# Kernel tuning notes

Measured on AMD Instinct MI355X. Metric: run time of the kernel, lower is better.

Reference implementation:

```python
import jax, jax.numpy as jnp
import numpy as np
import math

EMBED = 512
KDIM = 512
VDIM = 512
H = 8
HD = EMBED // H
N = 2048
L = 2048
B = 4


def setup_inputs() -> dict:
    key = jax.random.key(0)
    ks = jax.random.split(key, 14)
    s = 1.0 / math.sqrt(EMBED)
    return {
        "q": jax.random.normal(ks[0], (N, B, EMBED), jnp.float32),
        "k": jax.random.normal(ks[1], (L, B, KDIM), jnp.float32),
        "v": jax.random.normal(ks[2], (L, B, VDIM), jnp.float32),
        "pe1": jax.random.normal(ks[3], (B, N, 3), jnp.float32),
        "pe2": jax.random.normal(ks[4], (L, 3), jnp.float32),
        "Wq": jax.random.normal(ks[5], (EMBED, EMBED), jnp.float32) * s,
        "bq": jnp.zeros((EMBED,), jnp.float32),
        "Wk": jax.random.normal(ks[6], (EMBED, KDIM), jnp.float32) * s,
        "bk": jnp.zeros((EMBED,), jnp.float32),
        "Wv": jax.random.normal(ks[7], (EMBED, VDIM), jnp.float32) * s,
        "bv": jnp.zeros((EMBED,), jnp.float32),
        "Wo": jax.random.normal(ks[8], (EMBED, EMBED), jnp.float32) * s,
        "bo": jnp.zeros((EMBED,), jnp.float32),
    }


def reference(q, k, v, pe1, pe2, Wq, bq, Wk, bk, Wv, bv, Wo, bo):
    n, b, _ = q.shape
    l = k.shape[0]
    # projections (nn.Linear: x @ W.T + b)
    qp = q @ Wq.T + bq  # (n, b, E)
    kp = k @ Wk.T + bk  # (l, b, E)
    vp = v @ Wv.T + bv  # (l, b, E)
    # split heads -> (b, H, n, hd)
    qh = qp.reshape(n, b, H, HD).transpose(1, 2, 0, 3)
    kh = kp.reshape(l, b, H, HD).transpose(1, 2, 0, 3)
    vh = vp.reshape(l, b, H, HD).transpose(1, 2, 0, 3)
    # relative PE bias: (b, n, l), broadcast over heads
    pe_scores = jnp.einsum('bnc,lc->bnl', pe1, pe2)[:, None, :, :]
    scores = (jnp.einsum('bhnd,bhld->bhnl', qh, kh) + pe_scores) / math.sqrt(HD)
    attn = jax.nn.softmax(scores, axis=-1)
    out = jnp.einsum('bhnl,bhld->bhnd', attn, vh)  # (b, H, n, hd)
    out = out.transpose(2, 0, 1, 3).reshape(n, b, EMBED)
    return out @ Wo.T + bo
```

## Files before the change

kernel.cpp:

```cpp
#include <hip/hip_runtime.h>
#include <math.h>

#define EMBED 512
#define HDIM 64
#define NHEADS 8
#define SEQ_N 2048
#define SEQ_L 2048
#define BATCH 4
#define MROWS (SEQ_N*BATCH)
#define BE (BATCH*EMBED)

#define QSCALE 0.18033688f

typedef _Float16 f16;
typedef _Float16 half8 __attribute__((ext_vector_type(8)));
typedef _Float16 half4 __attribute__((ext_vector_type(4)));
typedef _Float16 half2v __attribute__((ext_vector_type(2)));
typedef float floatx4 __attribute__((ext_vector_type(4)));
typedef float floatx16 __attribute__((ext_vector_type(16)));

static __device__ inline float fast_exp2(float x) {
#if __has_builtin(__builtin_amdgcn_exp2f)
  return __builtin_amdgcn_exp2f(x);
#else
  return __expf(x * 0.69314718056f);
#endif
}

static __device__ inline half2v pk2(float a, float b) {
#if __has_builtin(__builtin_amdgcn_cvt_pkrtz)
  return __builtin_bit_cast(half2v, __builtin_amdgcn_cvt_pkrtz(a, b));
#else
  half2v o; o[0] = (f16)a; o[1] = (f16)b; return o;
#endif
}

static __device__ inline void gload16(const void* g, void* l) {
  __builtin_amdgcn_global_load_lds(
      (__attribute__((address_space(1))) void*)(g),
      (__attribute__((address_space(3))) void*)(l), 16, 0, 0);
}

__global__ __launch_bounds__(256) void cvt_all(const float* __restrict__ q,
                                               const float* __restrict__ k,
                                               const float* __restrict__ v,
                                               const float* __restrict__ Wq,
                                               const float* __restrict__ Wk,
                                               const float* __restrict__ Wv,
                                               const float* __restrict__ Wo,
                                               f16* __restrict__ qb, f16* __restrict__ kb,
                                               f16* __restrict__ vb, f16* __restrict__ Wb) {
  const long TOK = (long)MROWS * EMBED;
  const long WSZ = (long)EMBED * EMBED;
  int y = blockIdx.y;
  long i = ((long)blockIdx.x * 256 + threadIdx.x) * 4;
  if (y < 3) {
    if (i < TOK) {
      const float* s = y == 0 ? q : y == 1 ? k : v;
      f16* d = y == 0 ? qb : y == 1 ? kb : vb;
      float4 f = *reinterpret_cast<const float4*>(s + i);
      half4 o; o[0] = (f16)f.x; o[1] = (f16)f.y; o[2] = (f16)f.z; o[3] = (f16)f.w;
      *reinterpret_cast<half4*>(d + i) = o;
    }
  } else {
    if (i < 4 * WSZ) {
      int sel = (int)(i >> 18);
      long off = i & (WSZ - 1);
      const float* s = sel == 0 ? Wq : sel == 1 ? Wk : sel == 2 ? Wv : Wo;
      float4 f = *reinterpret_cast<const float4*>(s + off);
      half4 o; o[0] = (f16)f.x; o[1] = (f16)f.y; o[2] = (f16)f.z; o[3] = (f16)f.w;
      *reinterpret_cast<half4*>(Wb + i) = o;
    }
  }
}

__global__ __launch_bounds__(256) void gemm_qkv(const f16* __restrict__ A0,
                                                const f16* __restrict__ A1,
                                                const f16* __restrict__ A2,
                                                const f16* __restrict__ W0,
                                                const f16* __restrict__ W1,
                                                const f16* __restrict__ W2,
                                                const float* __restrict__ b0,
                                                const float* __restrict__ b1,
                                                const float* __restrict__ b2,
                                                f16* __restrict__ C0, f16* __restrict__ C1,
                                                f16* __restrict__ C2t) {
  __shared__ alignas(16) f16 As[128 * 32];
  __shared__ alignas(16) f16 Bs[128 * 32];
  const int sel = blockIdx.y >> 2;
  const f16* A = sel == 0 ? A0 : sel == 1 ? A1 : A2;
  const f16* Bt = sel == 0 ? W0 : sel == 1 ? W1 : W2;
  const float* bias = sel == 0 ? b0 : sel == 1 ? b1 : b2;
  const float scl = sel == 0 ? QSCALE : 1.0f;
  const int tid = threadIdx.x;
  const int wave = tid >> 6, lane = tid & 63, quad = lane >> 4, l16 = lane & 15;
  const int wm = wave & 1, wn = wave >> 1;
  const long m0 = (long)blockIdx.x * 128;
  const long n0 = (long)(blockIdx.y & 3) * 128;
  floatx4 acc[4][4] = {};
  const int srow = lane >> 2;
  const int scol = (lane & 3) * 8;

  for (int k0 = 0; k0 < EMBED; k0 += 32) {
    __syncthreads();
    gload16(A + (m0 + wave * 32 + srow) * EMBED + k0 + scol, &As[(wave * 32) * 32]);
    gload16(A + (m0 + wave * 32 + 16 + srow) * EMBED + k0 + scol, &As[(wave * 32 + 16) * 32]);
    gload16(Bt + (n0 + wave * 32 + srow) * EMBED + k0 + scol, &Bs[(wave * 32) * 32]);
    gload16(Bt + (n0 + wave * 32 + 16 + srow) * EMBED + k0 + scol, &Bs[(wave * 32 + 16) * 32]);
    __syncthreads();
    half8 af[4], bf[4];
#pragma unroll
    for (int i = 0; i < 4; ++i)
      af[i] = *reinterpret_cast<const half8*>(&As[(wm * 64 + i * 16 + l16) * 32 + quad * 8]);
#pragma unroll
    for (int j = 0; j < 4; ++j)
      bf[j] = *reinterpret_cast<const half8*>(&Bs[(wn * 64 + j * 16 + l16) * 32 + quad * 8]);
#pragma unroll
    for (int i = 0; i < 4; ++i)
#pragma unroll
      for (int j = 0; j < 4; ++j)
        acc[i][j] = __builtin_amdgcn_mfma_f32_16x16x32_f16(af[i], bf[j], acc[i][j], 0, 0, 0);
  }
#pragma unroll
  for (int i = 0; i < 4; ++i)
#pragma unroll
    for (int r = 0; r < 4; ++r) {
      long row = m0 + wm * 64 + i * 16 + quad * 4 + r;
#pragma unroll
      for (int j = 0; j < 4; ++j) {
        long col = n0 + wn * 64 + j * 16 + l16;
        float val = (acc[i][j][r] + bias[col]) * scl;
        if (sel == 2) {
          long bq = row & 3, ltok = row >> 2;
          long hh = col >> 6, dd = col & 63;
          C2t[(((bq << 3) + hh) * 64 + dd) * 2048 + ltok] = (f16)val;
        } else {
          f16* C = sel == 0 ? C0 : C1;
          C[row * EMBED + col] = (f16)val;
        }
      }
    }
}

__global__ __launch_bounds__(256) void gemm_out(const f16* __restrict__ A,
                                                const f16* __restrict__ Bt,
                                                const float* __restrict__ bias,
                                                float* __restrict__ C) {
  __shared__ alignas(16) f16 As[128 * 32];
  __shared__ alignas(16) f16 Bs[64 * 32];
  const int tid = threadIdx.x;
  const int wave = tid >> 6, lane = tid & 63, quad = lane >> 4, l16 = lane & 15;
  const long m0 = (long)blockIdx.x * 128;
  const long n0 = (long)blockIdx.y * 64;
  floatx4 acc[2][4] = {};
  const int srow = lane >> 2;
  const int scol = (lane & 3) * 8;

  for (int k0 = 0; k0 < EMBED; k0 += 32) {
    __syncthreads();
    gload16(A + (m0 + wave * 32 + srow) * EMBED + k0 + scol, &As[(wave * 32) * 32]);
    gload16(A + (m0 + wave * 32 + 16 + srow) * EMBED + k0 + scol, &As[(wave * 32 + 16) * 32]);
    gload16(Bt + (n0 + wave * 16 + srow) * EMBED + k0 + scol, &Bs[(wave * 16) * 32]);
    __syncthreads();
    half8 af[2], bf[4];
#pragma unroll
    for (int i = 0; i < 2; ++i)
      af[i] = *reinterpret_cast<const half8*>(&As[(wave * 32 + i * 16 + l16) * 32 + quad * 8]);
#pragma unroll
    for (int j = 0; j < 4; ++j)
      bf[j] = *reinterpret_cast<const half8*>(&Bs[(j * 16 + l16) * 32 + quad * 8]);
#pragma unroll
    for (int i = 0; i < 2; ++i)
#pragma unroll
      for (int j = 0; j < 4; ++j)
        acc[i][j] = __builtin_amdgcn_mfma_f32_16x16x32_f16(af[i], bf[j], acc[i][j], 0, 0, 0);
  }
#pragma unroll
  for (int i = 0; i < 2; ++i)
#pragma unroll
    for (int r = 0; r < 4; ++r) {
      long row = m0 + wave * 32 + i * 16 + quad * 4 + r;
#pragma unroll
      for (int j = 0; j < 4; ++j) {
        long col = n0 + j * 16 + l16;
        C[row * EMBED + col] = acc[i][j][r] + bias[col];
      }
    }
}

#define KST 88
#define VST 136
#define NCHUNK (SEQ_L / 128)
#define LDSB (128 * KST * 2 + 64 * VST * 2)
__global__ __launch_bounds__(512, 4) void attn_flash(const f16* __restrict__ qp,
                                                     const f16* __restrict__ kp,
                                                     const f16* __restrict__ vt,
                                                     const float* __restrict__ pe1,
                                                     const float* __restrict__ pe2,
                                                     f16* __restrict__ ao) {
  __shared__ alignas(16) unsigned char smem[LDSB];
  f16* Ks = reinterpret_cast<f16*>(smem);
  f16* Vt = reinterpret_cast<f16*>(smem + 128 * KST * 2);
  float* comb = reinterpret_cast<float*>(smem);
  const int tid = threadIdx.x, wave = tid >> 6, lane = tid & 63;
  const int m = lane & 31, h = lane >> 5;
  const int strip = wave & 3, half = wave >> 2;
  const int n0 = blockIdx.x * 128;
  const int b = blockIdx.y >> 3, hd = blockIdx.y & 7;
  const long headoff = (long)b * EMBED + hd * HDIM;
  const long vhead = (long)blockIdx.y * 64 * 2048;

  for (int c = tid; c < 1024; c += 512) {
    int r = c >> 3, col = (c & 7) * 8;
    *reinterpret_cast<uint4*>(&Ks[r * KST + col]) =
        *reinterpret_cast<const uint4*>(qp + (long)(n0 + r) * BE + headoff + col);
    int rv = c >> 4, cv = (c & 15) * 8;
    *reinterpret_cast<uint4*>(&Vt[rv * VST + cv]) =
        *reinterpret_cast<const uint4*>(vt + vhead + (long)rv * 2048 + 0 + cv);
  }
  {
    const uint4 z4 = {0, 0, 0, 0};
    const uint2 z2 = {0, 0};
    int r = tid >> 2, s = tid & 3;
    if (s == 0) *reinterpret_cast<uint2*>(&Ks[r * KST + 68]) = z2;
    else if (s == 1) *reinterpret_cast<uint4*>(&Ks[r * KST + 72]) = z4;
    else if (s == 2) *reinterpret_cast<uint4*>(&Ks[r * KST + 80]) = z4;
  }
  if (tid < 128) {
    long base = ((long)b * SEQ_N + n0 + tid) * 3;
    half4 v8;
    v8[0] = (f16)(pe1[base + 0] * QSCALE);
    v8[1] = (f16)(pe1[base + 1] * QSCALE);
    v8[2] = (f16)(pe1[base + 2] * QSCALE);
    v8[3] = (f16)0.f;
    *reinterpret_cast<half4*>(&Ks[tid * KST + 64]) = v8;
  }
  __syncthreads();

  half8 qf[5];
#pragma unroll
  for (int e = 0; e < 5; ++e)
    qf[e] = *reinterpret_cast<const half8*>(&Ks[(strip * 32 + m) * KST + e * 16 + h * 8]);
  __syncthreads();

  for (int c = tid; c < 1024; c += 512) {
    int r = c >> 3, col = (c & 7) * 8;
    *reinterpret_cast<uint4*>(&Ks[r * KST + col]) =
        *reinterpret_cast<const uint4*>(kp + (long)(0 + r) * BE + headoff + col);
  }
  if (tid < 128) {
    long bb = (long)(0 + tid) * 3;
    half4 p2;
    p2[0] = (f16)pe2[bb + 0]; p2[1] = (f16)pe2[bb + 1];
    p2[2] = (f16)pe2[bb + 2]; p2[3] = (f16)0.f;
    *reinterpret_cast<half4*>(&Ks[tid * KST + 64]) = p2;
  }

  floatx16 oacc[2] = {};
  float lpart = 0.f;

#pragma unroll 1
  for (int c = 0; c < NCHUNK; ++c) {
    __syncthreads();
#pragma unroll
    for (int tt = 0; tt < 2; ++tt) {
      const int t = half * 2 + tt;
      floatx16 st = {};
#pragma unroll
      for (int e = 0; e < 5; ++e) {
        half8 kf = *reinterpret_cast<const half8*>(&Ks[(t * 32 + m) * KST + e * 16 + h * 8]);
        st = __builtin_amdgcn_mfma_f32_32x32x16_f16(kf, qf[e], st, 0, 0, 0);
      }
      float p[16];
#pragma unroll
      for (int r = 0; r < 16; ++r) {
        p[r] = fast_exp2(st[r]);
        lpart += p[r];
      }
#pragma unroll
      for (int s = 0; s < 4; ++s) {
        half2v u0 = pk2(p[4 * s + 0], p[4 * s + 1]);
        half2v u1 = pk2(p[4 * s + 2], p[4 * s + 3]);
        half4 bp;
        bp[0] = u0[0]; bp[1] = u0[1]; bp[2] = u1[0]; bp[3] = u1[1];
        int lcol = t * 32 + s * 8 + h * 4;
#pragma unroll
        for (int dt = 0; dt < 2; ++dt) {
          half4 vf = *reinterpret_cast<const half4*>(&Vt[(dt * 32 + m) * VST + lcol]);
          oacc[dt] = __builtin_amdgcn_mfma_f32_32x32x8f16(vf, bp, oacc[dt], 0, 0, 0);
        }
      }
    }
    __syncthreads();
    if (c + 1 < NCHUNK) {
      const int l0 = (c + 1) * 128;
      for (int cc = tid; cc < 1024; cc += 512) {
        int r = cc >> 3, col = (cc & 7) * 8;
        *reinterpret_cast<uint4*>(&Ks[r * KST + col]) =
            *reinterpret_cast<const uint4*>(kp + (long)(l0 + r) * BE + headoff + col);
        int rv = cc >> 4, cv = (cc & 15) * 8;
        *reinterpret_cast<uint4*>(&Vt[rv * VST + cv]) =
            *reinterpret_cast<const uint4*>(vt + vhead + (long)rv * 2048 + l0 + cv);
      }
      if (tid < 128) {
        long bb = (long)(l0 + tid) * 3;
        half4 p2;
        p2[0] = (f16)pe2[bb + 0]; p2[1] = (f16)pe2[bb + 1];
        p2[2] = (f16)pe2[bb + 2]; p2[3] = (f16)0.f;
        *reinterpret_cast<half4*>(&Ks[tid * KST + 64]) = p2;
      }
    }
  }

  lpart += __shfl_xor(lpart, 32);

  if (half == 1) {
    float* dst = comb + (strip * 64 + lane) * 33;
#pragma unroll
    for (int dt = 0; dt < 2; ++dt)
#pragma unroll
      for (int x = 0; x < 16; ++x) dst[dt * 16 + x] = oacc[dt][x];
    dst[32] = lpart;
  }
  __syncthreads();
  if (half == 0) {
    const float* src = comb + (strip * 64 + lane) * 33;
#pragma unroll
    for (int dt = 0; dt < 2; ++dt)
#pragma unroll
      for (int x = 0; x < 16; ++x) oacc[dt][x] += src[dt * 16 + x];
    float inv = 1.f / (lpart + src[32]);
    long qrow = n0 + strip * 32 + m;
#pragma unroll
    for (int dt = 0; dt < 2; ++dt)
#pragma unroll
      for (int g = 0; g < 4; ++g) {
        half4 o4;
#pragma unroll
        for (int x = 0; x < 4; ++x) o4[x] = (f16)(oacc[dt][4 * g + x] * inv);
        int d = dt * 32 + 8 * g + 4 * h;
        *reinterpret_cast<half4*>(ao + qrow * BE + headoff + d) = o4;
      }
  }
}

extern "C" void kernel_launch(void* const* d_in, const int* in_sizes, int n_in,
                              void* d_out, int out_size, void* d_ws, size_t ws_size,
                              hipStream_t stream) {
  const float* q   = (const float*)d_in[0];
  const float* k   = (const float*)d_in[1];
  const float* v   = (const float*)d_in[2];
  const float* pe1 = (const float*)d_in[3];
  const float* pe2 = (const float*)d_in[4];
  const float* Wq  = (const float*)d_in[5];
  const float* bq  = (const float*)d_in[6];
  const float* Wk  = (const float*)d_in[7];
  const float* bk  = (const float*)d_in[8];
  const float* Wv  = (const float*)d_in[9];
  const float* bv  = (const float*)d_in[10];
  const float* Wo  = (const float*)d_in[11];
  const float* bo  = (const float*)d_in[12];
  float* out = (float*)d_out;

  f16* ws = (f16*)d_ws;
  const long TOK = (long)MROWS * EMBED;
  const long WSZ = (long)EMBED * EMBED;
  f16* qb  = ws;
  f16* kb  = qb + TOK;
  f16* vb  = kb + TOK;
  f16* Wqb = vb + TOK;
  f16* Wkb = Wqb + WSZ;
  f16* Wvb = Wkb + WSZ;
  f16* Wob = Wvb + WSZ;
  f16* qpb = Wob + WSZ;
  f16* kpb = qpb + TOK;
  f16* vtb = kpb + TOK;
  f16* aob = vtb + TOK;

  cvt_all<<<dim3(4096, 4), 256, 0, stream>>>(q, k, v, Wq, Wk, Wv, Wo, qb, kb, vb, Wqb);

  gemm_qkv<<<dim3(MROWS / 128, 12), 256, 0, stream>>>(qb, kb, vb, Wqb, Wkb, Wvb,
                                                      bq, bk, bv, qpb, kpb, vtb);

  attn_flash<<<dim3(SEQ_N / 128, BATCH * NHEADS), 512, 0, stream>>>(qpb, kpb, vtb, pe1, pe2, aob);

  gemm_out<<<dim3(MROWS / 128, EMBED / 64), 256, 0, stream>>>(aob, Wob, bo, out);
}
```

Measured before the change: 203.9 us.

## Double-buffer K/V tiles in attention and coalesce transposed V projection stores

The attention kernel now keeps two LDS buffers for K/V chunks and stages the next chunk before computing on the current one, removing one barrier per iteration and letting loads overlap compute. The QKV GEMM's transposed V output is first assembled in shared memory and then written with 16-byte vector stores instead of scattered 2-byte stores. The doubled LDS footprint in attention may reduce the number of resident blocks per CU, and the extra shared tile in the GEMM raises its LDS use.

Result: no change. 206.3 us (+1.2%).

```diff
diff --git a/kernel.cpp b/kernel.cpp
--- a/kernel.cpp
+++ b/kernel.cpp
@@ -74,6 +74,7 @@
   }
 }
 
+#define TST 136
 __global__ __launch_bounds__(256) void gemm_qkv(const f16* __restrict__ A0,
                                                 const f16* __restrict__ A1,
                                                 const f16* __restrict__ A2,
@@ -87,6 +88,7 @@
                                                 f16* __restrict__ C2t) {
   __shared__ alignas(16) f16 As[128 * 32];
   __shared__ alignas(16) f16 Bs[128 * 32];
+  __shared__ alignas(16) f16 Ts[128 * TST];
   const int sel = blockIdx.y >> 2;
   const f16* A = sel == 0 ? A0 : sel == 1 ? A1 : A2;
   const f16* Bt = sel == 0 ? W0 : sel == 1 ? W1 : W2;
@@ -121,25 +123,47 @@
       for (int j = 0; j < 4; ++j)
         acc[i][j] = __builtin_amdgcn_mfma_f32_16x16x32_f16(af[i], bf[j], acc[i][j], 0, 0, 0);
   }
-#pragma unroll
-  for (int i = 0; i < 4; ++i)
-#pragma unroll
-    for (int r = 0; r < 4; ++r) {
-      long row = m0 + wm * 64 + i * 16 + quad * 4 + r;
-#pragma unroll
-      for (int j = 0; j < 4; ++j) {
-        long col = n0 + wn * 64 + j * 16 + l16;
-        float val = (acc[i][j][r] + bias[col]) * scl;
-        if (sel == 2) {
-          long bq = row & 3, ltok = row >> 2;
-          long hh = col >> 6, dd = col & 63;
-          C2t[(((bq << 3) + hh) * 64 + dd) * 2048 + ltok] = (f16)val;
-        } else {
-          f16* C = sel == 0 ? C0 : C1;
-          C[row * EMBED + col] = (f16)val;
+
+  if (sel == 2) {
+#pragma unroll
+    for (int i = 0; i < 4; ++i)
+#pragma unroll
+      for (int r = 0; r < 4; ++r) {
+        int ltok = wm * 16 + i * 4 + quad;
+#pragma unroll
+        for (int j = 0; j < 4; ++j) {
+          int col = wn * 64 + j * 16 + l16;
+          float val = acc[i][j][r] + bias[n0 + col];
+          Ts[col * TST + r * 32 + ltok] = (f16)val;
         }
       }
-    }
+    __syncthreads();
+    const long ltok0 = m0 >> 2;
+    for (int e = tid; e < 512; e += 256) {
+      int col = e >> 2, bq = e & 3;
+      long gcol = n0 + col;
+      long hh = gcol >> 6, dd = gcol & 63;
+      const f16* src = &Ts[col * TST + bq * 32];
+      f16* dst = C2t + ((((long)bq << 3) + hh) * 64 + dd) * 2048 + ltok0;
+#pragma unroll
+      for (int x = 0; x < 4; ++x)
+        *reinterpret_cast<uint4*>(dst + x * 8) =
+            *reinterpret_cast<const uint4*>(src + x * 8);
+    }
+  } else {
+    f16* C = sel == 0 ? C0 : C1;
+#pragma unroll
+    for (int i = 0; i < 4; ++i)
+#pragma unroll
+      for (int r = 0; r < 4; ++r) {
+        long row = m0 + wm * 64 + i * 16 + quad * 4 + r;
+#pragma unroll
+        for (int j = 0; j < 4; ++j) {
+          long col = n0 + wn * 64 + j * 16 + l16;
+          C[row * EMBED + col] = (f16)((acc[i][j][r] + bias[col]) * scl);
+        }
+      }
+  }
 }
 
 __global__ __launch_bounds__(256) void gemm_out(const f16* __restrict__ A,
@@ -191,16 +215,14 @@
 #define KST 88
 #define VST 136
 #define NCHUNK (SEQ_L / 128)
-#define LDSB (128 * KST * 2 + 64 * VST * 2)
+#define BUFE (128 * KST + 64 * VST)
 __global__ __launch_bounds__(512, 4) void attn_flash(const f16* __restrict__ qp,
                                                      const f16* __restrict__ kp,
                                                      const f16* __restrict__ vt,
                                                      const float* __restrict__ pe1,
                                                      const float* __restrict__ pe2,
                                                      f16* __restrict__ ao) {
-  __shared__ alignas(16) unsigned char smem[LDSB];
-  f16* Ks = reinterpret_cast<f16*>(smem);
-  f16* Vt = reinterpret_cast<f16*>(smem + 128 * KST * 2);
+  __shared__ alignas(16) f16 smem[2 * BUFE];
   float* comb = reinterpret_cast<float*>(smem);
   const int tid = threadIdx.x, wave = tid >> 6, lane = tid & 63;
   const int m = lane & 31, h = lane >> 5;
@@ -210,21 +232,23 @@
   const long headoff = (long)b * EMBED + hd * HDIM;
   const long vhead = (long)blockIdx.y * 64 * 2048;
 
+  f16* Ks0 = smem;
   for (int c = tid; c < 1024; c += 512) {
     int r = c >> 3, col = (c & 7) * 8;
-    *reinterpret_cast<uint4*>(&Ks[r * KST + col]) =
+    *reinterpret_cast<uint4*>(&Ks0[r * KST + col]) =
         *reinterpret_cast<const uint4*>(qp + (long)(n0 + r) * BE + headoff + col);
-    int rv = c >> 4, cv = (c & 15) * 8;
-    *reinterpret_cast<uint4*>(&Vt[rv * VST + cv]) =
-        *reinterpret_cast<const uint4*>(vt + vhead + (long)rv * 2048 + 0 + cv);
   }
   {
     const uint4 z4 = {0, 0, 0, 0};
     const uint2 z2 = {0, 0};
     int r = tid >> 2, s = tid & 3;
-    if (s == 0) *reinterpret_cast<uint2*>(&Ks[r * KST + 68]) = z2;
-    else if (s == 1) *reinterpret_cast<uint4*>(&Ks[r * KST + 72]) = z4;
-    else if (s == 2) *reinterpret_cast<uint4*>(&Ks[r * KST + 80]) = z4;
+#pragma unroll
+    for (int bb = 0; bb < 2; ++bb) {
+      f16* Kb = smem + bb * BUFE;
+      if (s == 0) *reinterpret_cast<uint2*>(&Kb[r * KST + 68]) = z2;
+      else if (s == 1) *reinterpret_cast<uint4*>(&Kb[r * KST + 72]) = z4;
+      else if (s == 2) *reinterpret_cast<uint4*>(&Kb[r * KST + 80]) = z4;
+    }
   }
   if (tid < 128) {
     long base = ((long)b * SEQ_N + n0 + tid) * 3;
@@ -233,35 +257,47 @@
     v8[1] = (f16)(pe1[base + 1] * QSCALE);
     v8[2] = (f16)(pe1[base + 2] * QSCALE);
     v8[3] = (f16)0.f;
-    *reinterpret_cast<half4*>(&Ks[tid * KST + 64]) = v8;
+    *reinterpret_cast<half4*>(&Ks0[tid * KST + 64]) = v8;
   }
   __syncthreads();
 
   half8 qf[5];
 #pragma unroll
   for (int e = 0; e < 5; ++e)
-    qf[e] = *reinterpret_cast<const half8*>(&Ks[(strip * 32 + m) * KST + e * 16 + h * 8]);
+    qf[e] = *reinterpret_cast<const half8*>(&Ks0[(strip * 32 + m) * KST + e * 16 + h * 8]);
   __syncthreads();
 
-  for (int c = tid; c < 1024; c += 512) {
-    int r = c >> 3, col = (c & 7) * 8;
-    *reinterpret_cast<uint4*>(&Ks[r * KST + col]) =
-        *reinterpret_cast<const uint4*>(kp + (long)(0 + r) * BE + headoff + col);
-  }
-  if (tid < 128) {
-    long bb = (long)(0 + tid) * 3;
-    half4 p2;
-    p2[0] = (f16)pe2[bb + 0]; p2[1] = (f16)pe2[bb + 1];
-    p2[2] = (f16)pe2[bb + 2]; p2[3] = (f16)0.f;
-    *reinterpret_cast<half4*>(&Ks[tid * KST + 64]) = p2;
-  }
+  auto stage = [&](int l0, f16* KsD, f16* VtD) {
+    for (int c = tid; c < 1024; c += 512) {
+      int r = c >> 3, col = (c & 7) * 8;
+      *reinterpret_cast<uint4*>(&KsD[r * KST + col]) =
+          *reinterpret_cast<const uint4*>(kp + (long)(l0 + r) * BE + headoff + col);
+      int rv = c >> 4, cv = (c & 15) * 8;
+      *reinterpret_cast<uint4*>(&VtD[rv * VST + cv]) =
+          *reinterpret_cast<const uint4*>(vt + vhead + (long)rv * 2048 + l0 + cv);
+    }
+    if (tid < 128) {
+      long bb = (long)(l0 + tid) * 3;
+      half4 p2;
+      p2[0] = (f16)pe2[bb + 0]; p2[1] = (f16)pe2[bb + 1];
+      p2[2] = (f16)pe2[bb + 2]; p2[3] = (f16)0.f;
+      *reinterpret_cast<half4*>(&KsD[tid * KST + 64]) = p2;
+    }
+  };
+  stage(0, smem, smem + 128 * KST);
+  __syncthreads();
 
   floatx16 oacc[2] = {};
   float lpart = 0.f;
 
 #pragma unroll 1
   for (int c = 0; c < NCHUNK; ++c) {
-    __syncthreads();
+    if (c + 1 < NCHUNK) {
+      f16* nb = smem + ((c + 1) & 1) * BUFE;
+      stage((c + 1) * 128, nb, nb + 128 * KST);
+    }
+    const f16* Ks = smem + (c & 1) * BUFE;
+    const f16* Vt = Ks + 128 * KST;
 #pragma unroll
     for (int tt = 0; tt < 2; ++tt) {
       const int t = half * 2 + tt;
@@ -292,24 +328,6 @@
       }
     }
     __syncthreads();
-    if (c + 1 < NCHUNK) {
-      const int l0 = (c + 1) * 128;
-      for (int cc = tid; cc < 1024; cc += 512) {
-        int r = cc >> 3, col = (cc & 7) * 8;
-        *reinterpret_cast<uint4*>(&Ks[r * KST + col]) =
-            *reinterpret_cast<const uint4*>(kp + (long)(l0 + r) * BE + headoff + col);
-        int rv = cc >> 4, cv = (cc & 15) * 8;
-        *reinterpret_cast<uint4*>(&Vt[rv * VST + cv]) =
-            *reinterpret_cast<const uint4*>(vt + vhead + (long)rv * 2048 + l0 + cv);
-      }
-      if (tid < 128) {
-        long bb = (long)(l0 + tid) * 3;
-        half4 p2;
-        p2[0] = (f16)pe2[bb + 0]; p2[1] = (f16)pe2[bb + 1];
-        p2[2] = (f16)pe2[bb + 2]; p2[3] = (f16)0.f;
-        *reinterpret_cast<half4*>(&Ks[tid * KST + 64]) = p2;
-      }
-    }
   }
 
   lpart += __shfl_xor(lpart, 32);
```
